# Kernel optimization log

Hardware: AMD Instinct MI355X
Metric: run time of the kernel (lower is better)

The kernel has to match this reference:

```python
import jax, jax.numpy as jnp
import numpy as np

EPS = 1e-5

def _conv(x, w, pad):
    return jax.lax.conv_general_dilated(
        x, w, window_strides=(1, 1), padding=((pad, pad), (pad, pad)),
        dimension_numbers=('NCHW', 'OIHW', 'NCHW'))

def _dyn_branch(x, w, d):
    # x: [N,C,H,W]; w: [N,9,H,W] softmax weights; d: dilation.
    # Equivalent to unfold(k=3, dilation=d, padding=d) + bmm with w,
    # done as 9 shifted zero-padded slices (row-major kernel order).
    N, C, H, W = x.shape
    xp = jnp.pad(x, ((0, 0), (0, 0), (d, d), (d, d)))
    out = jnp.zeros_like(x)
    k = 0
    for dy in (-d, 0, d):
        for dx in (-d, 0, d):
            patch = xp[:, :, d + dy:d + dy + H, d + dx:d + dx + W]
            out = out + patch * w[:, k:k + 1]
            k += 1
    return out

def setup_inputs() -> dict:
    key = jax.random.key(0)
    k1, k2, k3 = jax.random.split(key, 3)
    C = 256
    x = jax.random.normal(k1, (2, C, 96, 96), dtype=jnp.float32)
    W_cat = jax.random.normal(k2, (45, C, 3, 3), dtype=jnp.float32) * 0.05
    W_scale = jax.random.normal(k3, (C, 6 * C, 1, 1), dtype=jnp.float32) * 0.05
    gamma = jnp.ones((C,), dtype=jnp.float32)
    beta = jnp.zeros((C,), dtype=jnp.float32)
    return {"x": x, "W_cat": W_cat, "W_scale": W_scale, "gamma": gamma, "beta": beta}

def reference(x, W_cat, W_scale, gamma, beta):
    guidance = _conv(x, W_cat, pad=1)  # [N,45,H,W]
    outs = [x]
    for i, d in enumerate((1, 6, 12, 24, 36)):
        w = jax.nn.softmax(guidance[:, 9 * i:9 * (i + 1)], axis=1)  # [N,9,H,W]
        outs.append(_dyn_branch(x, w, d))
    cat = jnp.concatenate(outs, axis=1)  # [N, 6C, H, W]
    y = _conv(cat, W_scale, pad=0)       # [N, C, H, W]
    # BatchNorm2d in training mode (batch statistics, biased variance)
    mean = jnp.mean(y, axis=(0, 2, 3), keepdims=True)
    var = jnp.var(y, axis=(0, 2, 3), keepdims=True)
    y = (y - mean) * jax.lax.rsqrt(var + EPS)
    return y * gamma[None, :, None, None] + beta[None, :, None, None]
```

## Files before the change

kernel.cpp:

```cpp
#include <hip/hip_runtime.h>

typedef __bf16 bf16x8 __attribute__((ext_vector_type(8)));
typedef float f32x4 __attribute__((ext_vector_type(4)));

#define HW 9216
#define ZSTR 176
#define ZSLAB 16896

__device__ __forceinline__ unsigned short f2bf(float f) {
  unsigned u = __float_as_uint(f);
  unsigned r = (u + 0x7FFFu + ((u >> 16) & 1u)) >> 16;
  return (unsigned short)r;
}
__device__ __forceinline__ float bf2f(unsigned short h) {
  return __uint_as_float(((unsigned)h) << 16);
}

__device__ __forceinline__ void async16(const unsigned short* g, unsigned short* l) {
  __builtin_amdgcn_global_load_lds(
      (const __attribute__((address_space(1))) unsigned int*)g,
      (__attribute__((address_space(3))) unsigned int*)l, 16, 0, 0);
}

template <int O>
__device__ __forceinline__ void tapfma(float* y, uint4 lo, uint4 hi, uint4 wv) {
  const unsigned short* lu = (const unsigned short*)&lo;
  const unsigned short* hu = (const unsigned short*)&hi;
  const unsigned short* wu = (const unsigned short*)&wv;
#pragma unroll
  for (int j = 0; j < 8; ++j) {
    unsigned short zz = (O + j < 8) ? lu[O + j] : hu[O + j - 8];
    y[j] += bf2f(wu[j]) * bf2f(zz);
  }
}

template <int B, int D>
__device__ __forceinline__ void branch9(float* y, const unsigned short* zslab,
                                        const unsigned short* gb, int h, int w0) {
#define TAPK(K, DY, DX)                                                       \
  {                                                                           \
    int hh = h + (DY);                                                        \
    int hc = min(max(hh, 0), 95);                                             \
    const unsigned short* zr = zslab + hc * ZSTR;                             \
    constexpr int O = (40 + (DX)) & 7;                                        \
    int eb = 40 + w0 + (DX)-O;                                                \
    uint4 lo = *(const uint4*)(zr + eb);                                      \
    uint4 hi = *(const uint4*)(zr + eb + 8);                                  \
    uint4 wv = *(const uint4*)(gb + (size_t)(((B - 1) * 9 + (K)) * 2) * HW);  \
    if ((unsigned)hh >= 96u) wv = make_uint4(0u, 0u, 0u, 0u);                 \
    tapfma<O>(y, lo, hi, wv);                                                 \
  }
  TAPK(0, -D, -D) TAPK(1, -D, 0) TAPK(2, -D, D)
  TAPK(3, 0, -D)  TAPK(4, 0, 0)  TAPK(5, 0, D)
  TAPK(6, D, -D)  TAPK(7, D, 0)  TAPK(8, D, D)
#undef TAPK
}

__global__ __launch_bounds__(256) void init_all(const float* __restrict__ x,
                                                const float* __restrict__ Ws,
                                                const float* __restrict__ Wc,
                                                unsigned short* __restrict__ xb,
                                                unsigned short* __restrict__ Wsb,
                                                unsigned short* __restrict__ Wcb,
                                                unsigned short* __restrict__ z) {
  __shared__ float tile[64][65];
  int id = blockIdx.x;
  int t = threadIdx.x;
  if (id < 1152) {
    int bx = id % 144, by = (id / 144) % 4, n = id / 576;
    int p0 = bx * 64, ci0 = by * 64;
    int cl = t & 63, q = t >> 6;
#pragma unroll
    for (int i = 0; i < 16; ++i) {
      int cir = q + i * 4;
      tile[cir][cl] = x[((size_t)(n * 256 + ci0 + cir)) * HW + p0 + cl];
    }
    __syncthreads();
#pragma unroll
    for (int i = 0; i < 16; ++i) {
      int pr = q + i * 4;
      xb[((size_t)(n * HW + p0 + pr)) * 256 + ci0 + cl] = f2bf(tile[cl][pr]);
    }
  } else if (id < 3120) {
    int u = (id - 1152) * 256 + t;
    if (u < 393216) {
      int j = u >> 8, k = u & 255;
      int co = j & 255, b = j >> 8;
      Wsb[u] = f2bf(Ws[(size_t)co * 1536 + b * 256 + k]);
    } else {
      int v = u - 393216;
      if (v < 110592) {
        int co = v / 2304, r = v % 2304;
        int j = r >> 8, ci = r & 255;
        Wcb[v] = (co < 45) ? f2bf(Wc[(size_t)co * 2304 + ci * 9 + j]) : (unsigned short)0;
      }
    }
  } else {
    int r = (id - 3120) * 256 + t;
    unsigned short* base = z + (size_t)r * ZSTR;
    uint4 zero = make_uint4(0u, 0u, 0u, 0u);
#pragma unroll
    for (int i = 0; i < 5; ++i) *(uint4*)(base + i * 8) = zero;
#pragma unroll
    for (int i = 0; i < 5; ++i) *(uint4*)(base + 136 + i * 8) = zero;
  }
}

__global__ __launch_bounds__(256) void gemms(const unsigned short* __restrict__ xb,
                                             const unsigned short* __restrict__ Wsb,
                                             const unsigned short* __restrict__ Wcb,
                                             unsigned short* __restrict__ z,
                                             unsigned short* __restrict__ gsmb) {
  __shared__ unsigned short smem[16384];
  int id = blockIdx.x;
  int t = threadIdx.x;
  int wid = t >> 6, lane = t & 63;
  int q = lane >> 4, ln = lane & 15;

  if (id < 288) {
    unsigned short* As = smem;
    unsigned short* Bs = smem + 4096;
    int m0 = id * 64;
    int mm = t >> 2, kq = t & 3;
    int m = m0 + mm;
    int img = m / HW, p = m % HW;
    int h = p / 96, w = p % 96;
    int mbase = img * HW;
    int nn = t >> 2;
    f32x4 acc[3] = {};
    uint4 aA0, aA1, aB0, aB1;

    {
      int hh = h - 1, ww = w - 1;
      bool valid = ((unsigned)hh < 96u) & ((unsigned)ww < 96u);
      const unsigned short* pa = xb + (size_t)(mbase + hh * 96 + ww) * 256 + kq * 8;
      aA0 = valid ? *(const uint4*)pa : make_uint4(0, 0, 0, 0);
      aA1 = valid ? *(const uint4*)(pa + 32) : make_uint4(0, 0, 0, 0);
      if (t < 192) {
        const unsigned short* pb = Wcb + (size_t)nn * 2304 + kq * 8;
        aB0 = *(const uint4*)pb;
        aB1 = *(const uint4*)(pb + 32);
      }
    }

    for (int s = 0; s < 36; ++s) {
      ((uint4*)As)[kq * 64 + mm] = aA0;
      ((uint4*)As)[(kq + 4) * 64 + mm] = aA1;
      if (t < 192) {
        ((uint4*)Bs)[kq * 48 + nn] = aB0;
        ((uint4*)Bs)[(kq + 4) * 48 + nn] = aB1;
      }
      __syncthreads();
      if (s + 1 < 36) {
        int s1 = s + 1;
        int j = s1 >> 2;
        int hh = h + j / 3 - 1, ww = w + j % 3 - 1;
        bool valid = ((unsigned)hh < 96u) & ((unsigned)ww < 96u);
        const unsigned short* pa =
            xb + (size_t)(mbase + hh * 96 + ww) * 256 + (s1 & 3) * 64 + kq * 8;
        aA0 = valid ? *(const uint4*)pa : make_uint4(0, 0, 0, 0);
        aA1 = valid ? *(const uint4*)(pa + 32) : make_uint4(0, 0, 0, 0);
        if (t < 192) {
          const unsigned short* pb = Wcb + (size_t)nn * 2304 + s1 * 64 + kq * 8;
          aB0 = *(const uint4*)pb;
          aB1 = *(const uint4*)(pb + 32);
        }
      }
#pragma unroll
      for (int kk = 0; kk < 2; ++kk) {
        bf16x8 a = ((const bf16x8*)As)[(kk * 4 + q) * 64 + wid * 16 + ln];
#pragma unroll
        for (int fn = 0; fn < 3; ++fn) {
          bf16x8 b = ((const bf16x8*)Bs)[(kk * 4 + q) * 48 + fn * 16 + ln];
          acc[fn] = __builtin_amdgcn_mfma_f32_16x16x32_bf16(a, b, acc[fn], 0, 0, 0);
        }
      }
      __syncthreads();
    }

    float* LDSf = (float*)smem;
#pragma unroll
    for (int fn = 0; fn < 3; ++fn)
#pragma unroll
      for (int r = 0; r < 4; ++r)
        LDSf[(wid * 16 + q * 4 + r) * 49 + fn * 16 + ln] = acc[fn][r];
    __syncthreads();
    if (t < 64) {
      const float* row = LDSf + t * 49;
      int mg = m0 + t;
      int img2 = mg / HW, p2 = mg - img2 * HW;
      for (int grp = 0; grp < 5; ++grp) {
        float v[9], mx = -1e30f;
#pragma unroll
        for (int k = 0; k < 9; ++k) { v[k] = row[grp * 9 + k]; mx = fmaxf(mx, v[k]); }
        float sum = 0.f;
#pragma unroll
        for (int k = 0; k < 9; ++k) { v[k] = __expf(v[k] - mx); sum += v[k]; }
        float inv = 1.f / sum;
#pragma unroll
        for (int k = 0; k < 9; ++k) {
          int col = grp * 9 + k;
          gsmb[((size_t)(col * 2 + img2)) * HW + p2] = f2bf(v[k] * inv);
        }
      }
    }
  } else {
    int zid = id - 288;
    int m0 = (zid % 144) * 128, c0 = (zid / 144) * 128;
    int wm = (wid >> 1) * 64, wn = (wid & 1) * 64;
    int half = wid & 1;
    const unsigned short* gbase =
        (wid < 2) ? xb + (size_t)(m0 + half * 64 + lane) * 256
                  : Wsb + (size_t)(c0 + half * 64 + lane) * 256;
    unsigned short* lbase0 = (wid < 2) ? smem : smem + 8192;
    f32x4 acc[4][4] = {};

#pragma unroll
    for (int kq = 0; kq < 4; ++kq)
      async16(gbase + kq * 8, lbase0 + (kq * 2 + half) * 512);
    __syncthreads();

    for (int s = 0; s < 8; ++s) {
      int cur = s & 1, nxt = cur ^ 1;
      if (s < 7) {
        int k0 = (s + 1) * 32;
#pragma unroll
        for (int kq = 0; kq < 4; ++kq)
          async16(gbase + k0 + kq * 8, lbase0 + nxt * 4096 + (kq * 2 + half) * 512);
      }
      const unsigned short* Asc = smem + cur * 4096;
      const unsigned short* Bsc = smem + 8192 + cur * 4096;
      bf16x8 a[4], b[4];
#pragma unroll
      for (int f = 0; f < 4; ++f) {
        a[f] = ((const bf16x8*)Asc)[q * 128 + wm + f * 16 + ln];
        b[f] = ((const bf16x8*)Bsc)[q * 128 + wn + f * 16 + ln];
      }
#pragma unroll
      for (int fm = 0; fm < 4; ++fm)
#pragma unroll
        for (int fn = 0; fn < 4; ++fn)
          acc[fm][fn] = __builtin_amdgcn_mfma_f32_16x16x32_bf16(a[fm], b[fn], acc[fm][fn], 0, 0, 0);
      __syncthreads();
    }

    int sl = c0 >> 8, cb = c0 & 255;
    int img = m0 / HW;
    int pbase = m0 - img * HW;
#pragma unroll
    for (int fm = 0; fm < 4; ++fm) {
      int p = pbase + wm + fm * 16 + q * 4;
      int hh = p / 96, ww = p % 96;
#pragma unroll
      for (int fn = 0; fn < 4; ++fn) {
        int ch = cb + wn + fn * 16 + ln;
        size_t slab = ((size_t)(sl * 256 + ch) * 2 + img) * ZSLAB;
        unsigned lo = (unsigned)f2bf(acc[fm][fn][0]) | ((unsigned)f2bf(acc[fm][fn][1]) << 16);
        unsigned hi = (unsigned)f2bf(acc[fm][fn][2]) | ((unsigned)f2bf(acc[fm][fn][3]) << 16);
        *(uint2*)(z + slab + hh * ZSTR + 40 + ww) = make_uint2(lo, hi);
      }
    }
  }
}

__global__ __launch_bounds__(384) void accum_chw(const unsigned short* __restrict__ z,
                                                 const unsigned short* __restrict__ gsmb,
                                                 float* __restrict__ yacc,
                                                 float* __restrict__ stats) {
  __shared__ float red[12];
  int t = threadIdx.x;
  int wq = t % 12, hl = t / 12;
  int h = blockIdx.x * 32 + hl;
  int img = blockIdx.y, ch = blockIdx.z;
  int w0 = wq * 8;
  int p0 = h * 96 + w0;
  const unsigned short* gb = gsmb + (size_t)img * HW + p0;

  float y[8] = {0.f, 0.f, 0.f, 0.f, 0.f, 0.f, 0.f, 0.f};
  {
    const unsigned short* zs = z + ((size_t)(ch * 2 + img)) * ZSLAB;
    uint4 v = *(const uint4*)(zs + h * ZSTR + 40 + w0);
    const unsigned short* u = (const unsigned short*)&v;
#pragma unroll
    for (int j = 0; j < 8; ++j) y[j] += bf2f(u[j]);
  }
  size_t chslab = (size_t)(ch * 2 + img) * ZSLAB;
  branch9<1, 1>(y, z + (size_t)(1 * 512) * ZSLAB + chslab, gb, h, w0);
  branch9<2, 6>(y, z + (size_t)(2 * 512) * ZSLAB + chslab, gb, h, w0);
  branch9<3, 12>(y, z + (size_t)(3 * 512) * ZSLAB + chslab, gb, h, w0);
  branch9<4, 24>(y, z + (size_t)(4 * 512) * ZSLAB + chslab, gb, h, w0);
  branch9<5, 36>(y, z + (size_t)(5 * 512) * ZSLAB + chslab, gb, h, w0);

  size_t ybase = ((size_t)(img * 256 + ch)) * HW + p0;
  *(float4*)(yacc + ybase) = make_float4(y[0], y[1], y[2], y[3]);
  *(float4*)(yacc + ybase + 4) = make_float4(y[4], y[5], y[6], y[7]);

  float s1 = 0.f, s2 = 0.f;
#pragma unroll
  for (int j = 0; j < 8; ++j) { s1 += y[j]; s2 += y[j] * y[j]; }
#pragma unroll
  for (int off = 1; off <= 32; off <<= 1) {
    s1 += __shfl_xor(s1, off);
    s2 += __shfl_xor(s2, off);
  }
  int wid = t >> 6, lane = t & 63;
  if (lane == 0) { red[wid] = s1; red[6 + wid] = s2; }
  __syncthreads();
  if (t == 0) {
    float a = red[0] + red[1] + red[2] + red[3] + red[4] + red[5];
    atomicAdd(&stats[ch], a);
  } else if (t == 64) {
    float b = red[6] + red[7] + red[8] + red[9] + red[10] + red[11];
    atomicAdd(&stats[256 + ch], b);
  }
}

__global__ __launch_bounds__(256) void bn_apply(const float* __restrict__ yacc,
                                                const float* __restrict__ stats,
                                                const float* __restrict__ gamma,
                                                const float* __restrict__ beta,
                                                float* __restrict__ out) {
  int q = blockIdx.x * 256 + threadIdx.x;
  int ch = (q / 2304) & 255;
  const float inv_cnt = 1.f / 18432.f;
  float mean = stats[ch] * inv_cnt;
  float var = stats[256 + ch] * inv_cnt - mean * mean;
  float sc = rsqrtf(var + 1e-5f) * gamma[ch];
  float sh = beta[ch] - mean * sc;
  float4 v = *(const float4*)(yacc + (size_t)q * 4);
  float4 o = make_float4(v.x * sc + sh, v.y * sc + sh, v.z * sc + sh, v.w * sc + sh);
  *(float4*)(out + (size_t)q * 4) = o;
}

extern "C" void kernel_launch(void* const* d_in, const int* in_sizes, int n_in,
                              void* d_out, int out_size, void* d_ws, size_t ws_size,
                              hipStream_t stream) {
  const float* x = (const float*)d_in[0];
  const float* Wc = (const float*)d_in[1];
  const float* Ws = (const float*)d_in[2];
  const float* gamma = (const float*)d_in[3];
  const float* beta = (const float*)d_in[4];
  float* out = (float*)d_out;

  unsigned short* xb = (unsigned short*)d_ws;
  unsigned short* Wsb = xb + 4718592;
  unsigned short* Wcb = Wsb + 393216;
  unsigned short* gsmb = Wcb + 110592;
  unsigned short* z = gsmb + 829440;
  float* yacc = (float*)(z + 51904512);
  float* stats = yacc + 4718592;

  hipMemsetAsync(stats, 0, 512 * sizeof(float), stream);
  init_all<<<4272, 256, 0, stream>>>(x, Ws, Wc, xb, Wsb, Wcb, z);
  gemms<<<2016, 256, 0, stream>>>(xb, Wsb, Wcb, z, gsmb);
  accum_chw<<<dim3(3, 2, 256), 384, 0, stream>>>(z, gsmb, yacc, stats);
  bn_apply<<<4608, 256, 0, stream>>>(yacc, stats, gamma, beta, out);
}
```

Before: 206.5 us.

## Store bf16 activations and weights in 128-row k-blocked tiles for contiguous async loads

The prep kernel now writes the transposed bf16 activations and the scale weights in a tiled layout: 128-row tiles, each holding 8-channel chunks contiguous across rows. The guidance-conv gather and the main GEMM's async global-to-LDS loads index this layout, so each wave's 16-byte loads for one k-chunk cover a contiguous 1 KB span instead of rows strided by 512 bytes. The aim is better coalescing of the global_load_lds traffic and of the prep-kernel stores, which now write full 16-byte vectors. In exchange, the conv gather's 3x3 shifted rows become scattered within tiles, and the parts not shown that read xb must also agree with the new layout.

```diff
diff --git a/kernel.cpp b/kernel.cpp
--- a/kernel.cpp
+++ b/kernel.cpp
@@ -6,6 +6,7 @@
 #define HW 9216
 #define ZSTR 176
 #define ZSLAB 16896
+#define XTILE 32768
 
 __device__ __forceinline__ unsigned short f2bf(float f) {
   unsigned u = __float_as_uint(f);
@@ -76,22 +77,32 @@
       tile[cir][cl] = x[((size_t)(n * 256 + ci0 + cir)) * HW + p0 + cl];
     }
     __syncthreads();
-#pragma unroll
-    for (int i = 0; i < 16; ++i) {
-      int pr = q + i * 4;
-      xb[((size_t)(n * HW + p0 + pr)) * 256 + ci0 + cl] = f2bf(tile[cl][pr]);
+    int R = n * HW + p0 + cl;
+    int Rt = R >> 7, Rl = R & 127;
+#pragma unroll
+    for (int i = 0; i < 2; ++i) {
+      int cloc = q * 2 + i;
+      unsigned rr[4];
+#pragma unroll
+      for (int jj = 0; jj < 4; ++jj) {
+        unsigned short a = f2bf(tile[cloc * 8 + jj * 2][cl]);
+        unsigned short b = f2bf(tile[cloc * 8 + jj * 2 + 1][cl]);
+        rr[jj] = (unsigned)a | ((unsigned)b << 16);
+      }
+      *(uint4*)(xb + (size_t)Rt * XTILE + (by * 8 + cloc) * 1024 + Rl * 8) =
+          make_uint4(rr[0], rr[1], rr[2], rr[3]);
     }
   } else if (id < 3120) {
     int u = (id - 1152) * 256 + t;
     if (u < 393216) {
-      int j = u >> 8, k = u & 255;
-      int co = j & 255, b = j >> 8;
-      Wsb[u] = f2bf(Ws[(size_t)co * 1536 + b * 256 + k]);
+      int r = u >> 8, k = u & 255;
+      Wsb[(size_t)(r >> 7) * XTILE + (k >> 3) * 1024 + (r & 127) * 8 + (k & 7)] =
+          f2bf(Ws[(size_t)(r & 255) * 1536 + (r >> 8) * 256 + k]);
     } else {
       int v = u - 393216;
       if (v < 110592) {
-        int co = v / 2304, r = v % 2304;
-        int j = r >> 8, ci = r & 255;
+        int co = v / 2304, rr = v % 2304;
+        int j = rr >> 8, ci = rr & 255;
         Wcb[v] = (co < 45) ? f2bf(Wc[(size_t)co * 2304 + ci * 9 + j]) : (unsigned short)0;
       }
     }
@@ -133,9 +144,11 @@
     {
       int hh = h - 1, ww = w - 1;
       bool valid = ((unsigned)hh < 96u) & ((unsigned)ww < 96u);
-      const unsigned short* pa = xb + (size_t)(mbase + hh * 96 + ww) * 256 + kq * 8;
+      int R = mbase + hh * 96 + ww;
+      const unsigned short* pa =
+          xb + (long)(R >> 7) * XTILE + kq * 1024 + (R & 127) * 8;
       aA0 = valid ? *(const uint4*)pa : make_uint4(0, 0, 0, 0);
-      aA1 = valid ? *(const uint4*)(pa + 32) : make_uint4(0, 0, 0, 0);
+      aA1 = valid ? *(const uint4*)(pa + 4096) : make_uint4(0, 0, 0, 0);
       if (t < 192) {
         const unsigned short* pb = Wcb + (size_t)nn * 2304 + kq * 8;
         aB0 = *(const uint4*)pb;
@@ -156,10 +169,11 @@
         int j = s1 >> 2;
         int hh = h + j / 3 - 1, ww = w + j % 3 - 1;
         bool valid = ((unsigned)hh < 96u) & ((unsigned)ww < 96u);
-        const unsigned short* pa =
-            xb + (size_t)(mbase + hh * 96 + ww) * 256 + (s1 & 3) * 64 + kq * 8;
+        int R = mbase + hh * 96 + ww;
+        const unsigned short* pa = xb + (long)(R >> 7) * XTILE +
+                                   ((s1 & 3) * 8 + kq) * 1024 + (R & 127) * 8;
         aA0 = valid ? *(const uint4*)pa : make_uint4(0, 0, 0, 0);
-        aA1 = valid ? *(const uint4*)(pa + 32) : make_uint4(0, 0, 0, 0);
+        aA1 = valid ? *(const uint4*)(pa + 4096) : make_uint4(0, 0, 0, 0);
         if (t < 192) {
           const unsigned short* pb = Wcb + (size_t)nn * 2304 + s1 * 64 + kq * 8;
           aB0 = *(const uint4*)pb;
@@ -206,27 +220,28 @@
     }
   } else {
     int zid = id - 288;
-    int m0 = (zid % 144) * 128, c0 = (zid / 144) * 128;
+    int mt = zid % 144, ct = zid / 144;
+    int m0 = mt * 128, c0 = ct * 128;
     int wm = (wid >> 1) * 64, wn = (wid & 1) * 64;
-    int half = wid & 1;
-    const unsigned short* gbase =
-        (wid < 2) ? xb + (size_t)(m0 + half * 64 + lane) * 256
-                  : Wsb + (size_t)(c0 + half * 64 + lane) * 256;
-    unsigned short* lbase0 = (wid < 2) ? smem : smem + 8192;
+    bool isB = wid >= 2;
+    const unsigned short* gsrc =
+        (isB ? Wsb + (size_t)ct * XTILE : xb + (size_t)mt * XTILE) + lane * 8;
+    unsigned short* lb = smem + (isB ? 8192 : 0);
+    int ow = (wid & 1) * 4;
     f32x4 acc[4][4] = {};
 
 #pragma unroll
     for (int kq = 0; kq < 4; ++kq)
-      async16(gbase + kq * 8, lbase0 + (kq * 2 + half) * 512);
+      async16(gsrc + (ow + kq) * 512, lb + (ow + kq) * 512);
     __syncthreads();
 
     for (int s = 0; s < 8; ++s) {
       int cur = s & 1, nxt = cur ^ 1;
       if (s < 7) {
-        int k0 = (s + 1) * 32;
 #pragma unroll
         for (int kq = 0; kq < 4; ++kq)
-          async16(gbase + k0 + kq * 8, lbase0 + nxt * 4096 + (kq * 2 + half) * 512);
+          async16(gsrc + (s + 1) * 4096 + (ow + kq) * 512,
+                  lb + nxt * 4096 + (ow + kq) * 512);
       }
       const unsigned short* Asc = smem + cur * 4096;
       const unsigned short* Bsc = smem + 8192 + cur * 4096;
```

Measured after the change: 193.1 us. 6.5% less time.
